# Optimization experiments

Hardware: AMD Instinct MI355X
Metric: run time of the kernel (lower is better)

## Reference

```python
import jax, jax.numpy as jnp
import numpy as np

B, N, CIN, H, E = 1, 20000, 128, 128, 320000


def setup_inputs() -> dict:
    key = jax.random.key(0)
    ks = jax.random.split(key, 16)
    x = jax.random.normal(ks[0], (B, N, CIN), jnp.float32)
    edge_index = jax.random.randint(ks[1], (2, E), 0, N, dtype=jnp.int64)
    edge_weight = jax.random.uniform(ks[2], (E,), jnp.float32)
    h = jax.random.normal(ks[3], (B, N, H), jnp.float32)
    c = jax.random.normal(ks[4], (B, N, H), jnp.float32)
    # GCN stack params, gate order [i, f, c, o]; 2 layers each (K=2)
    Wx0 = jax.random.normal(ks[5], (4, CIN, H), jnp.float32) / np.float32(np.sqrt(CIN))
    bx0 = jnp.zeros((4, H), jnp.float32)
    Wx1 = jax.random.normal(ks[6], (4, H, H), jnp.float32) / np.float32(np.sqrt(H))
    bx1 = jnp.zeros((4, H), jnp.float32)
    Wh0 = jax.random.normal(ks[7], (4, H, H), jnp.float32) / np.float32(np.sqrt(H))
    bh0 = jnp.zeros((4, H), jnp.float32)
    Wh1 = jax.random.normal(ks[8], (4, H, H), jnp.float32) / np.float32(np.sqrt(H))
    bh1 = jnp.zeros((4, H), jnp.float32)
    wc = jax.random.normal(ks[9], (3, H), jnp.float32) * 0.1  # peephole [i, f, o]
    bg = jnp.zeros((4, H), jnp.float32)  # gate biases [i, f, c, o]
    return dict(x=x, edge_index=edge_index, edge_weight=edge_weight, h=h, c=c,
                Wx0=Wx0, bx0=bx0, Wx1=Wx1, bx1=bx1,
                Wh0=Wh0, bh0=bh0, Wh1=Wh1, bh1=bh1, wc=wc, bg=bg)


def reference(x, edge_index, edge_weight, h, c,
              Wx0, bx0, Wx1, bx1, Wh0, bh0, Wh1, bh1, wc, bg):
    n = x.shape[1]
    src, dst = edge_index[0], edge_index[1]
    loop = jnp.arange(n)
    src2 = jnp.concatenate([src, loop])
    dst2 = jnp.concatenate([dst, loop])
    w2 = jnp.concatenate([edge_weight, jnp.ones((n,), edge_weight.dtype)])
    deg = jax.ops.segment_sum(w2, dst2, num_segments=n)
    dis = jnp.where(deg > 0, jax.lax.rsqrt(jnp.maximum(deg, 1e-12)), 0.0)
    norm = dis[src2] * w2 * dis[dst2]  # sym GCN norm with self loops

    def prop(t):  # t: [..., N, F] -> D^-1/2 (A+I) D^-1/2 t
        lead = t.shape[:-2]
        tf = t.reshape((-1,) + t.shape[-2:])
        m = tf[:, src2, :] * norm[None, :, None]
        agg = jax.vmap(lambda mm: jax.ops.segment_sum(mm, dst2, num_segments=n))(m)
        return agg.reshape(lead + agg.shape[-2:])

    def gcn4(t, W0, b0, W1, b1):  # 2-layer GCN, 4 gates at once
        a = prop(t)  # shared first aggregation: [B,N,F]
        h0 = jax.nn.relu(jnp.einsum('bnc,gch->gbnh', a, W0) + b0[:, None, None, :])
        a1 = prop(h0)  # [4,B,N,H]
        return jnp.einsum('gbnh,ghk->gbnk', a1, W1) + b1[:, None, None, :]

    G = gcn4(x, Wx0, bx0, Wx1, bx1) + gcn4(h, Wh0, bh0, Wh1, bh1)  # [4,B,N,H]
    I = jax.nn.sigmoid(G[0] + wc[0] * c + bg[0])
    F = jax.nn.sigmoid(G[1] + wc[1] * c + bg[1])
    T = jnp.tanh(G[2] + bg[2])
    Cn = F * c + I * T
    O = jax.nn.sigmoid(G[3] + wc[2] * Cn + bg[3])
    Hn = O * jnp.tanh(Cn)
    return (Hn, Cn)
```

## Files before the change

### kernel.cpp

```cpp
#include <hip/hip_runtime.h>
#include <hip/hip_bf16.h>
#include <stdint.h>

#define NN    20000
#define NP    20096
#define EE    320000
#define CH    128
#define GC    512
#define NHtot 2560000

typedef short bf16x8 __attribute__((ext_vector_type(8)));
typedef float f32x4  __attribute__((ext_vector_type(4)));

__device__ __forceinline__ unsigned short f2bf(float f) {
    __hip_bfloat16 b = __float2bfloat16(f);
    union { __hip_bfloat16 b; unsigned short u; } c; c.b = b; return c.u;
}
__device__ __forceinline__ void fma8(uint4 u, float n, float* acc) {
    union { unsigned int i; float f; } t;
    t.i = u.x << 16;         acc[0] += n * t.f;
    t.i = u.x & 0xffff0000u; acc[1] += n * t.f;
    t.i = u.y << 16;         acc[2] += n * t.f;
    t.i = u.y & 0xffff0000u; acc[3] += n * t.f;
    t.i = u.z << 16;         acc[4] += n * t.f;
    t.i = u.z & 0xffff0000u; acc[5] += n * t.f;
    t.i = u.w << 16;         acc[6] += n * t.f;
    t.i = u.w & 0xffff0000u; acc[7] += n * t.f;
}
__device__ __forceinline__ void tof8(uint4 u, float* f) {
    union { unsigned int i; float f; } t;
    t.i = u.x << 16;         f[0] = t.f;
    t.i = u.x & 0xffff0000u; f[1] = t.f;
    t.i = u.y << 16;         f[2] = t.f;
    t.i = u.y & 0xffff0000u; f[3] = t.f;
    t.i = u.z << 16;         f[4] = t.f;
    t.i = u.z & 0xffff0000u; f[5] = t.f;
    t.i = u.w << 16;         f[6] = t.f;
    t.i = u.w & 0xffff0000u; f[7] = t.f;
}
__device__ __forceinline__ uint2 pack4(const float* f) {
    uint2 v;
    v.x = (unsigned int)f2bf(f[0]) | ((unsigned int)f2bf(f[1]) << 16);
    v.y = (unsigned int)f2bf(f[2]) | ((unsigned int)f2bf(f[3]) << 16);
    return v;
}
__device__ __forceinline__ uint4 pack8(const float* f) {
    uint4 v;
    v.x = (unsigned int)f2bf(f[0]) | ((unsigned int)f2bf(f[1]) << 16);
    v.y = (unsigned int)f2bf(f[2]) | ((unsigned int)f2bf(f[3]) << 16);
    v.z = (unsigned int)f2bf(f[4]) | ((unsigned int)f2bf(f[5]) << 16);
    v.w = (unsigned int)f2bf(f[6]) | ((unsigned int)f2bf(f[7]) << 16);
    return v;
}
__device__ __forceinline__ void gload_lds16(const void* g, void* l) {
    __builtin_amdgcn_global_load_lds(
        (const __attribute__((address_space(1))) void*)g,
        (__attribute__((address_space(3))) void*)l, 16, 0, 0);
}

__global__ void k_cntprep(const int* __restrict__ ei, int* __restrict__ cnt,
                          const float* __restrict__ W0, const float* __restrict__ W1,
                          const float* __restrict__ W2, const float* __restrict__ W3,
                          unsigned short* __restrict__ T0, unsigned short* __restrict__ T1,
                          unsigned short* __restrict__ T2, unsigned short* __restrict__ T3,
                          const float* __restrict__ bx1, const float* __restrict__ bh1,
                          const float* __restrict__ bg, float* __restrict__ btot) {
    int bid = blockIdx.x;
    if (bid < EE / 256) {
        int e = bid * 256 + threadIdx.x;
        atomicAdd(&cnt[ei[EE + e]], 1);
        return;
    }
    int pid = bid - EE / 256;
    int z = pid >> 8, y = (pid >> 6) & 3, xb = pid & 63;
    if (z == 0 && y == 0 && xb < 2) {
        int f = xb * 256 + threadIdx.x;
        btot[f] = bx1[f] + bh1[f] + bg[f];
    }
    const float* W; unsigned short* T;
    switch (z) {
        case 0:  W = W0; T = T0; break;
        case 1:  W = W1; T = T1; break;
        case 2:  W = W2; T = T2; break;
        default: W = W3; T = T3; break;
    }
    int n = xb * 2 + (threadIdx.x >> 7);
    int k = threadIdx.x & 127;
    T[((size_t)y * 128 + n) * 128 + k] = f2bf(W[((size_t)y * 128 + k) * 128 + n]);
}

__global__ void k_scan1(const int* __restrict__ cnt, int* __restrict__ rowoff,
                        int* __restrict__ bsum) {
    __shared__ int wsum[4];
    int i = blockIdx.x * 256 + threadIdx.x;
    int self = (i < NN) ? cnt[i] : 0;
    int lane = threadIdx.x & 63, wid = threadIdx.x >> 6;
    int v = self;
    #pragma unroll
    for (int off = 1; off < 64; off <<= 1) {
        int u = __shfl_up(v, off);
        if (lane >= off) v += u;
    }
    if (lane == 63) wsum[wid] = v;
    __syncthreads();
    int wof = 0;
    for (int k = 0; k < wid; ++k) wof += wsum[k];
    if (i < NN) rowoff[i] = wof + v - self;
    if (threadIdx.x == 255) bsum[blockIdx.x] = wof + v;
}

__global__ void k_scan2(int* __restrict__ bsum) {
    int lane = threadIdx.x;
    int base = 0;
    for (int start = 0; start < 80; start += 64) {
        int i = start + lane;
        int self = (i < 80) ? bsum[i] : 0;
        int v = self;
        #pragma unroll
        for (int off = 1; off < 64; off <<= 1) {
            int u = __shfl_up(v, off);
            if (lane >= off) v += u;
        }
        if (i < 80) bsum[i] = base + v - self;
        base += __shfl(v, 63);
    }
}

__global__ void k_scan3(int* __restrict__ rowoff, const int* __restrict__ bsum,
                        int* __restrict__ cur) {
    int i = blockIdx.x * 256 + threadIdx.x;
    if (i < NN) {
        int v = rowoff[i] + bsum[i >> 8];
        rowoff[i] = v; cur[i] = v;
    }
    if (i == NN) rowoff[NN] = EE;
}

__global__ void k_scatter(const int* __restrict__ ei, const float* __restrict__ ew,
                          int* __restrict__ cur, int2* __restrict__ csre) {
    int e = blockIdx.x * 256 + threadIdx.x;
    if (e >= EE) return;
    int s = ei[e], d = ei[EE + e];
    int p = atomicAdd(&cur[d], 1);
    csre[p] = make_int2(s, __float_as_int(ew[e]));
}

__global__ __launch_bounds__(256) void k_degcast(
        const float* __restrict__ x, const float* __restrict__ h,
        const int* __restrict__ rowoff, const int2* __restrict__ csre,
        float* __restrict__ dis, unsigned short* __restrict__ xhb) {
    int wid = threadIdx.x >> 6, lane = threadIdx.x & 63;
    int w = blockIdx.x * 4 + wid;
    int e0 = rowoff[w], e1 = rowoff[w + 1];
    float s = 0.f;
    for (int e = e0 + lane; e < e1; e += 64) s += __int_as_float(csre[e].y);
    #pragma unroll
    for (int off = 32; off; off >>= 1) s += __shfl_xor(s, off);
    float dn = rsqrtf(fmaxf(1.0f + s, 1e-12f));
    if (lane == 0) dis[w] = dn;
    const float* src = (lane < 32) ? x + (size_t)w * CH + lane * 4
                                   : h + (size_t)w * CH + (lane - 32) * 4;
    float4 v = *(const float4*)src;
    float f[4] = { dn * v.x, dn * v.y, dn * v.z, dn * v.w };
    *(uint2*)(xhb + (size_t)w * 256 + lane * 4) = pack4(f);
}

__global__ __launch_bounds__(256) void k_prop256m(
        const unsigned short* __restrict__ tab, unsigned short* __restrict__ o,
        const int* __restrict__ rowoff, const int2* __restrict__ csre,
        const float* __restrict__ dis) {
    int chunk = blockIdx.x & 3;
    int wbase = (blockIdx.x >> 2) * 32 + (threadIdx.x >> 6) * 8;
    int l = threadIdx.x & 63, grp = l >> 3, li = l & 7;
    int w = wbase + grp;
    const uint4* T4 = (const uint4*)tab;
    int coff = chunk * 8 + li;
    float acc[8];
    tof8(T4[(size_t)w * 32 + coff], acc);
    int e0 = rowoff[w], deg = rowoff[w + 1] - e0;
    int md = deg;
    md = max(md, __shfl_xor(md, 8));
    md = max(md, __shfl_xor(md, 16));
    md = max(md, __shfl_xor(md, 32));
    int k = 0;
    for (; k + 4 <= md; k += 4) {
        int2 p0 = csre[k     < deg ? e0 + k     : 0];
        int2 p1 = csre[k + 1 < deg ? e0 + k + 1 : 0];
        int2 p2 = csre[k + 2 < deg ? e0 + k + 2 : 0];
        int2 p3 = csre[k + 3 < deg ? e0 + k + 3 : 0];
        uint4 u0 = T4[(size_t)p0.x * 32 + coff];
        uint4 u1 = T4[(size_t)p1.x * 32 + coff];
        uint4 u2 = T4[(size_t)p2.x * 32 + coff];
        uint4 u3 = T4[(size_t)p3.x * 32 + coff];
        float n0 = (k     < deg) ? __int_as_float(p0.y) : 0.f;
        float n1 = (k + 1 < deg) ? __int_as_float(p1.y) : 0.f;
        float n2 = (k + 2 < deg) ? __int_as_float(p2.y) : 0.f;
        float n3 = (k + 3 < deg) ? __int_as_float(p3.y) : 0.f;
        fma8(u0, n0, acc); fma8(u1, n1, acc);
        fma8(u2, n2, acc); fma8(u3, n3, acc);
    }
    for (; k < md; ++k) {
        int2 p = csre[k < deg ? e0 + k : 0];
        float n = (k < deg) ? __int_as_float(p.y) : 0.f;
        fma8(T4[(size_t)p.x * 32 + coff], n, acc);
    }
    float dw = dis[w];
    #pragma unroll
    for (int j = 0; j < 8; ++j) acc[j] *= dw;
    ((uint4*)o)[(size_t)w * 32 + coff] = pack8(acc);
}

#define SWZ(r, c8) (((r) << 4) + ((c8) ^ ((r) & 15)))

__global__ __launch_bounds__(256) void k_gemm1(
        const unsigned short* __restrict__ A,
        const unsigned short* __restrict__ Wtx, const unsigned short* __restrict__ Wth,
        const float* __restrict__ bx0, const float* __restrict__ bh0,
        unsigned short* __restrict__ outx, unsigned short* __restrict__ outh) {
    __shared__ uint4 As[2048];
    __shared__ uint4 Bs[2048];
    const int side = blockIdx.z;
    const int aoff = side * 128;
    const unsigned short* Wt = side ? Wth : Wtx;
    const float* bias        = side ? bh0 : bx0;
    unsigned short* out      = side ? outh : outx;

    const int    g    = blockIdx.y;
    const size_t row0 = (size_t)blockIdx.x * 128;
    const int    t    = threadIdx.x;
    const int    wv   = t >> 6;
    const unsigned short* Wg = Wt + (size_t)g * 16384;

    #pragma unroll
    for (int p = 0; p < 8; ++p) {
        int id = t + 256 * p, r = id >> 4, cc = id & 15;
        int c8 = cc ^ (r & 15);
        gload_lds16(A + (row0 + r) * 256 + aoff + c8 * 8, &As[p * 256 + wv * 64]);
        gload_lds16(Wg + r * CH + c8 * 8,                 &Bs[p * 256 + wv * 64]);
    }
    __syncthreads();

    const int l = t & 63;
    const int m0 = (wv >> 1) * 64, n0 = (wv & 1) * 64;
    const int lm = l & 15, q = l >> 4;
    f32x4 acc[4][4];
    #pragma unroll
    for (int i = 0; i < 4; ++i)
        #pragma unroll
        for (int j = 0; j < 4; ++j) { acc[i][j][0]=0.f; acc[i][j][1]=0.f; acc[i][j][2]=0.f; acc[i][j][3]=0.f; }

    #pragma unroll
    for (int kc = 0; kc < 4; ++kc) {
        int c8 = kc * 4 + q;
        bf16x8 a[4], b[4];
        #pragma unroll
        for (int i = 0; i < 4; ++i) { int r = m0 + i * 16 + lm; a[i] = *(const bf16x8*)&As[SWZ(r, c8)]; }
        #pragma unroll
        for (int j = 0; j < 4; ++j) { int r = n0 + j * 16 + lm; b[j] = *(const bf16x8*)&Bs[SWZ(r, c8)]; }
        #pragma unroll
        for (int i = 0; i < 4; ++i)
            #pragma unroll
            for (int j = 0; j < 4; ++j)
                acc[i][j] = __builtin_amdgcn_mfma_f32_16x16x32_bf16(a[i], b[j], acc[i][j], 0, 0, 0);
    }

    #pragma unroll
    for (int j = 0; j < 4; ++j) {
        float bb = bias[g * CH + n0 + j * 16 + lm];
        #pragma unroll
        for (int i = 0; i < 4; ++i)
            #pragma unroll
            for (int r = 0; r < 4; ++r) {
                int rowl = m0 + i * 16 + q * 4 + r;
                int col  = n0 + j * 16 + lm;
                out[(row0 + rowl) * GC + g * CH + col] = f2bf(fmaxf(acc[i][j][r] + bb, 0.f));
            }
    }
}

__global__ __launch_bounds__(256) void k_gemm2(
        const unsigned short* __restrict__ A1, const unsigned short* __restrict__ A2,
        const unsigned short* __restrict__ Wt1, const unsigned short* __restrict__ Wt2,
        const float* __restrict__ dis, unsigned short* __restrict__ outS) {
    __shared__ uint4 As[2048];
    __shared__ uint4 Bs[2048];
    const int    g    = blockIdx.y;
    const size_t row0 = (size_t)blockIdx.x * 128;
    const int    t    = threadIdx.x;
    const int    wv   = t >> 6;
    const int l = t & 63;
    const int m0 = (wv >> 1) * 64, n0 = (wv & 1) * 64;
    const int lm = l & 15, q = l >> 4;
    f32x4 acc[4][4];
    #pragma unroll
    for (int i = 0; i < 4; ++i)
        #pragma unroll
        for (int j = 0; j < 4; ++j) { acc[i][j][0]=0.f; acc[i][j][1]=0.f; acc[i][j][2]=0.f; acc[i][j][3]=0.f; }

    for (int side = 0; side < 2; ++side) {
        if (side) __syncthreads();
        const unsigned short* Ap = side ? A2 : A1;
        const unsigned short* Wg = (side ? Wt2 : Wt1) + (size_t)g * 16384;
        #pragma unroll
        for (int p = 0; p < 8; ++p) {
            int id = t + 256 * p, r = id >> 4, cc = id & 15;
            int c8 = cc ^ (r & 15);
            gload_lds16(Ap + (row0 + r) * GC + g * CH + c8 * 8, &As[p * 256 + wv * 64]);
            gload_lds16(Wg + r * CH + c8 * 8,                   &Bs[p * 256 + wv * 64]);
        }
        __syncthreads();
        #pragma unroll
        for (int kc = 0; kc < 4; ++kc) {
            int c8 = kc * 4 + q;
            bf16x8 a[4], b[4];
            #pragma unroll
            for (int i = 0; i < 4; ++i) { int r = m0 + i * 16 + lm; a[i] = *(const bf16x8*)&As[SWZ(r, c8)]; }
            #pragma unroll
            for (int j = 0; j < 4; ++j) { int r = n0 + j * 16 + lm; b[j] = *(const bf16x8*)&Bs[SWZ(r, c8)]; }
            #pragma unroll
            for (int i = 0; i < 4; ++i)
                #pragma unroll
                for (int j = 0; j < 4; ++j)
                    acc[i][j] = __builtin_amdgcn_mfma_f32_16x16x32_bf16(a[i], b[j], acc[i][j], 0, 0, 0);
        }
    }

    #pragma unroll
    for (int j = 0; j < 4; ++j)
        #pragma unroll
        for (int i = 0; i < 4; ++i)
            #pragma unroll
            for (int r = 0; r < 4; ++r) {
                int rowl = m0 + i * 16 + q * 4 + r;
                int col  = n0 + j * 16 + lm;
                float dr = dis[row0 + rowl];
                outS[(row0 + rowl) * GC + g * CH + col] = f2bf(dr * acc[i][j][r]);
            }
}

__global__ __launch_bounds__(256) void k_prop512m(
        const unsigned short* __restrict__ Sb, float* __restrict__ Gbuf,
        const int* __restrict__ rowoff, const int2* __restrict__ csre,
        const float* __restrict__ dis) {
    int chunk = blockIdx.x & 7;
    int wbase = (blockIdx.x >> 3) * 32 + (threadIdx.x >> 6) * 8;
    int l = threadIdx.x & 63, grp = l >> 3, li = l & 7;
    int w = wbase + grp;
    const uint4* S4 = (const uint4*)Sb;
    int coff = chunk * 8 + li;
    float acc[8];
    tof8(S4[(size_t)w * 64 + coff], acc);
    int e0 = rowoff[w], deg = rowoff[w + 1] - e0;
    int md = deg;
    md = max(md, __shfl_xor(md, 8));
    md = max(md, __shfl_xor(md, 16));
    md = max(md, __shfl_xor(md, 32));
    int k = 0;
    for (; k + 4 <= md; k += 4) {
        int2 p0 = csre[k     < deg ? e0 + k     : 0];
        int2 p1 = csre[k + 1 < deg ? e0 + k + 1 : 0];
        int2 p2 = csre[k + 2 < deg ? e0 + k + 2 : 0];
        int2 p3 = csre[k + 3 < deg ? e0 + k + 3 : 0];
        uint4 u0 = S4[(size_t)p0.x * 64 + coff];
        uint4 u1 = S4[(size_t)p1.x * 64 + coff];
        uint4 u2 = S4[(size_t)p2.x * 64 + coff];
        uint4 u3 = S4[(size_t)p3.x * 64 + coff];
        float n0 = (k     < deg) ? __int_as_float(p0.y) : 0.f;
        float n1 = (k + 1 < deg) ? __int_as_float(p1.y) : 0.f;
        float n2 = (k + 2 < deg) ? __int_as_float(p2.y) : 0.f;
        float n3 = (k + 3 < deg) ? __int_as_float(p3.y) : 0.f;
        fma8(u0, n0, acc); fma8(u1, n1, acc);
        fma8(u2, n2, acc); fma8(u3, n3, acc);
    }
    for (; k < md; ++k) {
        int2 p = csre[k < deg ? e0 + k : 0];
        float n = (k < deg) ? __int_as_float(p.y) : 0.f;
        fma8(S4[(size_t)p.x * 64 + coff], n, acc);
    }
    float dw = dis[w];
    #pragma unroll
    for (int j = 0; j < 8; ++j) acc[j] *= dw;
    float* gp = Gbuf + (size_t)w * GC + chunk * 64 + li * 8;
    *(float4*)gp       = *(float4*)&acc[0];
    *(float4*)(gp + 4) = *(float4*)&acc[4];
}

__global__ __launch_bounds__(256) void k_lstm(
        const float* __restrict__ Gbuf, const float* __restrict__ c,
        const float* __restrict__ btot, const float* __restrict__ wc,
        float* __restrict__ out) {
    int t = threadIdx.x;
    int w = blockIdx.x * 2 + (t >> 7);
    int hh = t & 127;
    const float* gr = Gbuf + (size_t)w * GC;
    float g0 = gr[hh]       + btot[hh];
    float g1 = gr[128 + hh] + btot[128 + hh];
    float g2 = gr[256 + hh] + btot[256 + hh];
    float g3 = gr[384 + hh] + btot[384 + hh];
    float cv = c[(size_t)w * CH + hh];
    float I  = 1.f / (1.f + expf(-(g0 + wc[hh]       * cv)));
    float F  = 1.f / (1.f + expf(-(g1 + wc[128 + hh] * cv)));
    float T  = tanhf(g2);
    float Cn = F * cv + I * T;
    float O  = 1.f / (1.f + expf(-(g3 + wc[256 + hh] * Cn)));
    out[(size_t)w * CH + hh]         = O * tanhf(Cn);
    out[NHtot + (size_t)w * CH + hh] = Cn;
}

extern "C" void kernel_launch(void* const* d_in, const int* in_sizes, int n_in,
                              void* d_out, int out_size, void* d_ws, size_t ws_size,
                              hipStream_t stream) {
    (void)in_sizes; (void)n_in; (void)out_size; (void)ws_size;
    const float* x   = (const float*)d_in[0];
    const int*   ei  = (const int*)d_in[1];
    const float* ew  = (const float*)d_in[2];
    const float* h   = (const float*)d_in[3];
    const float* c   = (const float*)d_in[4];
    const float* Wx0 = (const float*)d_in[5];
    const float* bx0 = (const float*)d_in[6];
    const float* Wx1 = (const float*)d_in[7];
    const float* bx1 = (const float*)d_in[8];
    const float* Wh0 = (const float*)d_in[9];
    const float* bh0 = (const float*)d_in[10];
    const float* Wh1 = (const float*)d_in[11];
    const float* bh1 = (const float*)d_in[12];
    const float* wc  = (const float*)d_in[13];
    const float* bg  = (const float*)d_in[14];
    float* out = (float*)d_out;

    float* wsf  = (float*)d_ws;
    float* dis  = wsf;
    int*   cnt  = (int*)(wsf + 20480);
    int*   row  = (int*)(wsf + 40960);
    int*   cur  = (int*)(wsf + 61696);
    int*   bsum = (int*)(wsf + 82176);
    float* btot = wsf + 82432;
    int2*  csre = (int2*)(wsf + 82944);
    unsigned short* Wt0x = (unsigned short*)(wsf + 722944);
    unsigned short* Wt0h = (unsigned short*)(wsf + 755712);
    unsigned short* Wt1x = (unsigned short*)(wsf + 788480);
    unsigned short* Wt1h = (unsigned short*)(wsf + 821248);
    unsigned short* xhb  = (unsigned short*)(wsf + 854016);
    unsigned short* axh  = (unsigned short*)(wsf + 3426304);
    unsigned short* h0x  = (unsigned short*)(wsf + 5998592);
    unsigned short* h0h  = (unsigned short*)(wsf + 11143168);
    unsigned short* Sb   = (unsigned short*)(wsf + 16287744);
    float* Gbuf = wsf + 5998592;

    hipMemsetAsync(cnt, 0, 20480 * sizeof(int), stream);

    k_cntprep<<<EE / 256 + 1024, 256, 0, stream>>>(ei, cnt,
                                                   Wx0, Wh0, Wx1, Wh1,
                                                   Wt0x, Wt0h, Wt1x, Wt1h,
                                                   bx1, bh1, bg, btot);
    k_scan1  <<<80, 256, 0, stream>>>(cnt, row, bsum);
    k_scan2  <<<1, 64, 0, stream>>>(bsum);
    k_scan3  <<<80, 256, 0, stream>>>(row, bsum, cur);
    k_scatter<<<EE / 256, 256, 0, stream>>>(ei, ew, cur, csre);

    k_degcast<<<NN / 4, 256, 0, stream>>>(x, h, row, csre, dis, xhb);

    k_prop256m<<<(NN / 32) * 4, 256, 0, stream>>>(xhb, axh, row, csre, dis);

    dim3 g1(NP / 128, 4, 2);
    k_gemm1<<<g1, 256, 0, stream>>>(axh, Wt0x, Wt0h, bx0, bh0, h0x, h0h);
    dim3 g2(NP / 128, 4);
    k_gemm2<<<g2, 256, 0, stream>>>(h0x, h0h, Wt1x, Wt1h, dis, Sb);

    k_prop512m<<<(NN / 32) * 8, 256, 0, stream>>>(Sb, Gbuf, row, csre, dis);
    k_lstm<<<NN / 2, 256, 0, stream>>>(Gbuf, c, btot, wc, out);
}
```

Before: 256.9 us.

## Sort nodes by in-degree bins so propagation groups share similar degrees

Builds a degree-binned permutation of nodes (histogram in scan1, prefix in scan2, new k_perm kernel) and makes both propagation kernels process nodes in that order. Each 8-lane group inside a wavefront loops to the maximum degree of its peers, so grouping similar-degree nodes is meant to cut wasted padded iterations. The cost is an extra kernel, atomics on 64 bins, and the loss of locality between neighbouring node rows and output writes.

```diff
diff --git a/kernel.cpp b/kernel.cpp
--- a/kernel.cpp
+++ b/kernel.cpp
@@ -90,10 +90,11 @@
 }
 
 __global__ void k_scan1(const int* __restrict__ cnt, int* __restrict__ rowoff,
-                        int* __restrict__ bsum) {
+                        int* __restrict__ bsum, int* __restrict__ dbin) {
     __shared__ int wsum[4];
     int i = blockIdx.x * 256 + threadIdx.x;
     int self = (i < NN) ? cnt[i] : 0;
+    if (i < NN) atomicAdd(&dbin[min(self, 63)], 1);
     int lane = threadIdx.x & 63, wid = threadIdx.x >> 6;
     int v = self;
     #pragma unroll
@@ -109,7 +110,7 @@
     if (threadIdx.x == 255) bsum[blockIdx.x] = wof + v;
 }
 
-__global__ void k_scan2(int* __restrict__ bsum) {
+__global__ void k_scan2(int* __restrict__ bsum, int* __restrict__ dbin) {
     int lane = threadIdx.x;
     int base = 0;
     for (int start = 0; start < 80; start += 64) {
@@ -124,6 +125,14 @@
         if (i < 80) bsum[i] = base + v - self;
         base += __shfl(v, 63);
     }
+    int d = dbin[lane];
+    int v = d;
+    #pragma unroll
+    for (int off = 1; off < 64; off <<= 1) {
+        int u = __shfl_up(v, off);
+        if (lane >= off) v += u;
+    }
+    dbin[lane] = v - d;
 }
 
 __global__ void k_scan3(int* __restrict__ rowoff, const int* __restrict__ bsum,
@@ -134,6 +143,15 @@
         rowoff[i] = v; cur[i] = v;
     }
     if (i == NN) rowoff[NN] = EE;
+}
+
+__global__ void k_perm(const int* __restrict__ cnt, int* __restrict__ dbin,
+                       int* __restrict__ perm) {
+    int i = blockIdx.x * 256 + threadIdx.x;
+    if (i >= NN) return;
+    int b = min(cnt[i], 63);
+    int p = atomicAdd(&dbin[b], 1);
+    perm[p] = i;
 }
 
 __global__ void k_scatter(const int* __restrict__ ei, const float* __restrict__ ew,
@@ -168,11 +186,11 @@
 __global__ __launch_bounds__(256) void k_prop256m(
         const unsigned short* __restrict__ tab, unsigned short* __restrict__ o,
         const int* __restrict__ rowoff, const int2* __restrict__ csre,
-        const float* __restrict__ dis) {
+        const float* __restrict__ dis, const int* __restrict__ perm) {
     int chunk = blockIdx.x & 3;
     int wbase = (blockIdx.x >> 2) * 32 + (threadIdx.x >> 6) * 8;
     int l = threadIdx.x & 63, grp = l >> 3, li = l & 7;
-    int w = wbase + grp;
+    int w = perm[wbase + grp];
     const uint4* T4 = (const uint4*)tab;
     int coff = chunk * 8 + li;
     float acc[8];
@@ -341,11 +359,11 @@
 __global__ __launch_bounds__(256) void k_prop512m(
         const unsigned short* __restrict__ Sb, float* __restrict__ Gbuf,
         const int* __restrict__ rowoff, const int2* __restrict__ csre,
-        const float* __restrict__ dis) {
+        const float* __restrict__ dis, const int* __restrict__ perm) {
     int chunk = blockIdx.x & 7;
     int wbase = (blockIdx.x >> 3) * 32 + (threadIdx.x >> 6) * 8;
     int l = threadIdx.x & 63, grp = l >> 3, li = l & 7;
-    int w = wbase + grp;
+    int w = perm[wbase + grp];
     const uint4* S4 = (const uint4*)Sb;
     int coff = chunk * 8 + li;
     float acc[8];
@@ -434,6 +452,7 @@
     int*   row  = (int*)(wsf + 40960);
     int*   cur  = (int*)(wsf + 61696);
     int*   bsum = (int*)(wsf + 82176);
+    int*   dbin = bsum + 96;
     float* btot = wsf + 82432;
     int2*  csre = (int2*)(wsf + 82944);
     unsigned short* Wt0x = (unsigned short*)(wsf + 722944);
@@ -446,27 +465,30 @@
     unsigned short* h0h  = (unsigned short*)(wsf + 11143168);
     unsigned short* Sb   = (unsigned short*)(wsf + 16287744);
     float* Gbuf = wsf + 5998592;
+    int*   perm = (int*)(wsf + 21432320);
 
     hipMemsetAsync(cnt, 0, 20480 * sizeof(int), stream);
+    hipMemsetAsync(dbin, 0, 64 * sizeof(int), stream);
 
     k_cntprep<<<EE / 256 + 1024, 256, 0, stream>>>(ei, cnt,
                                                    Wx0, Wh0, Wx1, Wh1,
                                                    Wt0x, Wt0h, Wt1x, Wt1h,
                                                    bx1, bh1, bg, btot);
-    k_scan1  <<<80, 256, 0, stream>>>(cnt, row, bsum);
-    k_scan2  <<<1, 64, 0, stream>>>(bsum);
+    k_scan1  <<<80, 256, 0, stream>>>(cnt, row, bsum, dbin);
+    k_scan2  <<<1, 64, 0, stream>>>(bsum, dbin);
     k_scan3  <<<80, 256, 0, stream>>>(row, bsum, cur);
+    k_perm   <<<80, 256, 0, stream>>>(cnt, dbin, perm);
     k_scatter<<<EE / 256, 256, 0, stream>>>(ei, ew, cur, csre);
 
     k_degcast<<<NN / 4, 256, 0, stream>>>(x, h, row, csre, dis, xhb);
 
-    k_prop256m<<<(NN / 32) * 4, 256, 0, stream>>>(xhb, axh, row, csre, dis);
+    k_prop256m<<<(NN / 32) * 4, 256, 0, stream>>>(xhb, axh, row, csre, dis, perm);
 
     dim3 g1(NP / 128, 4, 2);
     k_gemm1<<<g1, 256, 0, stream>>>(axh, Wt0x, Wt0h, bx0, bh0, h0x, h0h);
     dim3 g2(NP / 128, 4);
     k_gemm2<<<g2, 256, 0, stream>>>(h0x, h0h, Wt1x, Wt1h, dis, Sb);
 
-    k_prop512m<<<(NN / 32) * 8, 256, 0, stream>>>(Sb, Gbuf, row, csre, dis);
+    k_prop512m<<<(NN / 32) * 8, 256, 0, stream>>>(Sb, Gbuf, row, csre, dis, perm);
     k_lstm<<<NN / 2, 256, 0, stream>>>(Gbuf, c, btot, wc, out);
 }
```

After: 363.5 us. 1.41x slower.
